# Kernel optimization log

Measured on AMD Instinct MI355X. Metric: run time of the kernel, lower is better.

The kernel has to match this reference:

```python
import jax, jax.numpy as jnp
import numpy as np

N = 48
E = N * (N - 1)
H_LSTM = 32
EPS = 20.0

def _conv1d(x, w, b):
    # x: [B, Cin, L], w: [Cout, Cin, K] -> [B, Cout, L], 'same' padding
    y = jax.lax.conv_general_dilated(x, w, window_strides=(1,), padding='SAME',
                                     dimension_numbers=('NCH', 'OIH', 'NCH'))
    return y + b[None, :, None]

def _map(M, x):
    # map_features: linear map along dim 0 (gather for n_to_e one-hot rows,
    # incidence-sum scatter for e_to_n). M: [O, I], x: [I, ...] -> [O, ...]
    return jnp.tensordot(M, x, axes=1)

def _node_cnn(x, adj, layers, final):
    # graph conv stack: neighbor mix (adj along dim 0) + conv1d over node axis + relu
    nl = len(layers)
    for i, (w, b) in enumerate(layers):
        x = _conv1d(_map(adj, x), w, b)
        if not (final and i == nl - 1):
            x = jax.nn.relu(x)
    return x

def _node_lstm(x, mem, adj, w, b):
    # mem = cat([c, h], dim=1); gates from conv over adj-mixed cat([x, h])
    H = mem.shape[1] // 2
    c, h = mem[:, :H], mem[:, H:]
    gates = _conv1d(_map(adj, jnp.concatenate([x, h], axis=1)), w, b)
    i, f, g, o = jnp.split(gates, 4, axis=1)
    c2 = jax.nn.sigmoid(f) * c + jax.nn.sigmoid(i) * jnp.tanh(g)
    h2 = jax.nn.sigmoid(o) * jnp.tanh(c2)
    return jnp.concatenate([c2, h2], axis=1)

def _forward(bi, bij, msgi, msgj, v, nmem0, emem0, neadj, eeadj,
             e_to_n0, e_to_n1, n_to_e0, n_to_e1, decoding, params):
    fm, efm, nlstm, elstm, pp, epp = params
    n = bi.shape[0]
    e = bij.shape[0]
    # map_node_feature_to_edge
    bi_g1 = _map(n_to_e0, bi)   # [E,1,N]
    bi_g2 = _map(n_to_e1, bi)   # [E,1,N]
    # softmax (logsumexp) message computation over bij [E,1,N,N]
    cmsgi = jax.nn.logsumexp((bi_g2[:, :, None, :] + bij) * EPS, axis=3) / EPS  # [E,1,N]
    cmsgj = jax.nn.logsumexp((bi_g1[:, :, :, None] + bij) * EPS, axis=2) / EPS  # [E,1,N]
    ncmsgi = _map(e_to_n0, cmsgi)
    ncmsgj = _map(e_to_n1, cmsgj)
    nnmsgi = _map(e_to_n0, msgi)
    nnmsgj = _map(e_to_n1, msgj)
    # partial_feature (detached in original)
    dec_mat = jax.nn.one_hot(decoding, n, dtype=bi.dtype)        # [N,N]
    xi = _map(n_to_e0, dec_mat)[:, :, None]                      # [E,N,1]
    xj = _map(n_to_e1, dec_mat)[:, None, :]                      # [E,1,N]
    ep = bij.reshape(e, n, n)
    f1 = jax.lax.stop_gradient(_map(e_to_n0, (ep * xi).sum(axis=1)).reshape(n, 1, n))
    f2 = jax.lax.stop_gradient(_map(e_to_n1, (ep * xj).sum(axis=2)).reshape(n, 1, n))
    node_feature = jnp.concatenate([bi, bi + v, nnmsgi, nnmsgj, ncmsgi, ncmsgj, f1, f2], axis=1)  # [N,8,N]
    edge_feature = jnp.concatenate([msgi, msgj, cmsgi, cmsgj, bi_g1, bi_g2], axis=1)              # [E,6,N]
    nfeat = _node_cnn(node_feature, neadj, fm, False)   # [N,32,N]
    efeat = _node_cnn(edge_feature, eeadj, efm, False)  # [E,32,N]
    ntoe1, ntoe2 = _map(n_to_e0, nfeat), _map(n_to_e1, nfeat)
    eton1, eton2 = _map(e_to_n0, efeat), _map(e_to_n1, efeat)
    nfeat = jnp.concatenate([nfeat, eton1, eton2], axis=1)  # [N,96,N]
    efeat = jnp.concatenate([efeat, ntoe1, ntoe2], axis=1)  # [E,96,N]
    nmem_new = _node_lstm(nfeat, nmem0, neadj, nlstm[0], nlstm[1])  # [N,64,N]
    emem_new = _node_lstm(efeat, emem0, eeadj, elstm[0], elstm[1])  # [E,64,N]
    nfeat = nmem_new[:, H_LSTM:]   # h part
    efeat = emem_new[:, H_LSTM:]
    ntoe1, ntoe2 = _map(n_to_e0, nfeat), _map(n_to_e1, nfeat)
    eton1, eton2 = _map(e_to_n0, efeat), _map(e_to_n1, efeat)
    nfeat = jnp.concatenate([nfeat, eton1, eton2], axis=1)
    efeat = jnp.concatenate([efeat, ntoe1, ntoe2], axis=1)
    efeat = _node_cnn(efeat, eeadj, epp, True)   # [E,2,N]
    nfeat = _node_cnn(nfeat, neadj, pp, True)    # [N,1,N]
    nmsgi = efeat[:, 0:1] + 0.5 * cmsgi - msgi
    nmsgj = efeat[:, 1:2] + 0.5 * cmsgj - msgj
    nv = nfeat.mean(axis=0, keepdims=True)       # [1,1,N]
    v_out = v + nv
    bij_out = bij - nmsgi.reshape(e, 1, n, 1) - nmsgj.reshape(e, 1, 1, n)
    bi_out = bi + _map(e_to_n0, nmsgi) + _map(e_to_n1, nmsgj) - nv
    msgi_out = msgi + nmsgi
    msgj_out = msgj + nmsgj
    # get_current_dual (softmax=True)
    cdual = (v_out.sum()
             + jax.nn.logsumexp(bi_out.reshape(-1, n) * EPS, axis=1).sum() / EPS
             + jax.nn.logsumexp(bij_out.reshape(-1, n * n) * EPS, axis=1).sum() / EPS)
    return bi_out, bij_out, msgi_out, msgj_out, v_out, cdual, nmem_new, emem_new, f1, f2

def setup_inputs() -> dict:
    key = jax.random.key(0)
    ks = jax.random.split(key, 16)
    ii, jj = np.meshgrid(np.arange(N), np.arange(N), indexing='ij')
    mask = ii != jj
    src, dst = ii[mask], jj[mask]  # [E] complete directed graph
    eye = np.eye(N, dtype=np.float32)
    n_to_e0 = jnp.asarray(eye[src])  # [E,N] one-hot gather
    n_to_e1 = jnp.asarray(eye[dst])
    e_to_n0 = n_to_e0.T              # [N,E] incidence scatter-sum
    e_to_n1 = n_to_e1.T
    def glorot(k, shape):
        fan_in = shape[1] * shape[2]
        return jax.random.normal(k, shape, jnp.float32) / np.sqrt(fan_in)
    pk = jax.random.split(ks[15], 20)
    return dict(
        bi=jax.random.normal(ks[0], (N, 1, N), jnp.float32),
        bij=jax.random.normal(ks[1], (E, 1, N, N), jnp.float32),
        msgi=jnp.zeros((E, 1, N), jnp.float32),
        msgj=jnp.zeros((E, 1, N), jnp.float32),
        v=jnp.zeros((1, 1, N), jnp.float32),
        nmem0=jnp.zeros((N, 2 * H_LSTM, N), jnp.float32),
        emem0=jnp.zeros((E, 2 * H_LSTM, N), jnp.float32),
        neadj=jax.random.uniform(ks[2], (N, N), jnp.float32) / N,
        eeadj=jax.random.uniform(ks[3], (E, E), jnp.float32) / E,
        e_to_n0=e_to_n0, e_to_n1=e_to_n1, n_to_e0=n_to_e0, n_to_e1=n_to_e1,
        decoding=jax.random.randint(ks[4], (N,), 0, N),
        fm_w0=glorot(pk[0], (32, 8, 3)), fm_b0=jnp.zeros((32,), jnp.float32),
        fm_w1=glorot(pk[1], (32, 32, 3)), fm_b1=jnp.zeros((32,), jnp.float32),
        efm_w0=glorot(pk[2], (32, 6, 3)), efm_b0=jnp.zeros((32,), jnp.float32),
        efm_w1=glorot(pk[3], (32, 32, 3)), efm_b1=jnp.zeros((32,), jnp.float32),
        nlstm_w=glorot(pk[4], (128, 128, 3)), nlstm_b=jnp.zeros((128,), jnp.float32),
        elstm_w=glorot(pk[5], (128, 128, 3)), elstm_b=jnp.zeros((128,), jnp.float32),
        pp_w0=glorot(pk[6], (16, 96, 3)), pp_b0=jnp.zeros((16,), jnp.float32),
        pp_w1=glorot(pk[7], (1, 16, 3)), pp_b1=jnp.zeros((1,), jnp.float32),
        epp_w0=glorot(pk[8], (16, 96, 3)), epp_b0=jnp.zeros((16,), jnp.float32),
        epp_w1=glorot(pk[9], (2, 16, 3)), epp_b1=jnp.zeros((2,), jnp.float32),
    )

def reference(bi, bij, msgi, msgj, v, nmem0, emem0, neadj, eeadj,
              e_to_n0, e_to_n1, n_to_e0, n_to_e1, decoding,
              fm_w0, fm_b0, fm_w1, fm_b1, efm_w0, efm_b0, efm_w1, efm_b1,
              nlstm_w, nlstm_b, elstm_w, elstm_b,
              pp_w0, pp_b0, pp_w1, pp_b1, epp_w0, epp_b0, epp_w1, epp_b1):
    params = ([(fm_w0, fm_b0), (fm_w1, fm_b1)],
              [(efm_w0, efm_b0), (efm_w1, efm_b1)],
              (nlstm_w, nlstm_b), (elstm_w, elstm_b),
              [(pp_w0, pp_b0), (pp_w1, pp_b1)],
              [(epp_w0, epp_b0), (epp_w1, epp_b1)])
    return _forward(bi, bij, msgi, msgj, v, nmem0, emem0, neadj, eeadj,
                    e_to_n0, e_to_n1, n_to_e0, n_to_e1, decoding, params)
```

## Files before the change

kernel.cpp:

```cpp
#include <hip/hip_runtime.h>
#include <cstdint>
#include <cstddef>

#define EE 2256
#define EP 2304

typedef __attribute__((ext_vector_type(8))) short bf16x8;
typedef __attribute__((ext_vector_type(4))) float f32x4;

__device__ __forceinline__ unsigned short f2b(float f){
  unsigned u = __builtin_bit_cast(unsigned, f);
  u += 0x7fffu + ((u>>16)&1u);
  return (unsigned short)(u>>16);
}
__device__ __forceinline__ float b2f(unsigned short h){
  unsigned u = ((unsigned)h)<<16; return __builtin_bit_cast(float, u);
}
__device__ __forceinline__ float sigm(float x){ return 1.f/(1.f+__expf(-x)); }
__device__ __forceinline__ float tanhfast(float x){ return 1.f - 2.f/(__expf(2.f*x)+1.f); }

typedef __attribute__((address_space(3))) unsigned int lds_u32;
typedef __attribute__((address_space(1))) const unsigned int gbl_u32;
__device__ __forceinline__ void glds16(const void* g, void* l){
  __builtin_amdgcn_global_load_lds((gbl_u32*)g, (lds_u32*)l, 16, 0, 0);
}

__global__ void gm_zero(float4* p, long n){
  long i = (long)blockIdx.x*blockDim.x + threadIdx.x;
  if (i < n) p[i] = make_float4(0.f,0.f,0.f,0.f);
}

__global__ void gm_prep_eeadj(const float* __restrict__ src, unsigned short* __restrict__ dst){
  int idx = blockIdx.x*256 + threadIdx.x;
  if (idx >= EP*EP) return;
  int r = idx / EP, k = idx - r*EP;
  float v = (r < EE && k < EE) ? src[(size_t)r*EE + k] : 0.f;
  dst[idx] = f2b(v);
}

__global__ void gm_prep_wconv(const float* __restrict__ w, unsigned short* __restrict__ dst,
                              int Co, int Cin, int KPT, int Kpad, int tot){
  int idx = blockIdx.x*256 + threadIdx.x;
  if (idx >= tot) return;
  int co = idx / Kpad; int k = idx - co*Kpad;
  int t = k / KPT; int ci = k - t*KPT;
  float v = (co < Co && t < 3 && ci < Cin) ? w[((size_t)co*Cin + ci)*3 + t] : 0.f;
  dst[idx] = f2b(v);
}

__global__ __launch_bounds__(256) void gm_cmsg(const float* __restrict__ bi, const float* __restrict__ bij,
                                               float* __restrict__ cmi, float* __restrict__ cmj){
  int e = blockIdx.x; int tid = threadIdx.x;
  __shared__ float t[48*49]; __shared__ float bs[48], bd[48];
  const float* src = bij + (size_t)e*2304;
  for (int i=tid;i<2304;i+=256){ int r=i/48, c=i-r*48; t[r*49+c]=src[i]; }
  if (tid<48){ int s=e/47, m=e-s*47; int d=m+(m>=s); bs[tid]=bi[s*48+tid]; bd[tid]=bi[d*48+tid]; }
  __syncthreads();
  if (tid < 48){
    float mx=-1e30f;
    for (int n=0;n<48;n++) mx = fmaxf(mx, t[tid*49+n]+bd[n]);
    float sm=0.f;
    for (int n=0;n<48;n++) sm += __expf((t[tid*49+n]+bd[n]-mx)*20.f);
    cmi[e*48+tid] = mx + __logf(sm)*(1.f/20.f);
  } else if (tid>=64 && tid<112){
    int n = tid-64;
    float mx=-1e30f;
    for (int k=0;k<48;k++) mx = fmaxf(mx, t[k*49+n]+bs[k]);
    float sm=0.f;
    for (int k=0;k<48;k++) sm += __expf((t[k*49+n]+bs[k]-mx)*20.f);
    cmj[e*48+n] = mx + __logf(sm)*(1.f/20.f);
  }
}

__global__ __launch_bounds__(256) void gm_node_accum(const float* __restrict__ bij, const float* __restrict__ cmi,
                              const float* __restrict__ cmj, const float* __restrict__ msgi,
                              const float* __restrict__ msgj, const int* __restrict__ dec,
                              float* ncmi, float* ncmj, float* nnmi, float* nnmj,
                              float* o_f1, float* o_f2){
  int i = blockIdx.x; int tid = threadIdx.x;
  __shared__ float red[5][6][48];
  int mg = tid / 48;
  int w  = tid - mg*48;
  if (mg < 5){
    int dc = dec[i];
    float a1=0,a2=0,a3=0,a4=0,s1=0,s2=0;
    for (int m=mg; m<47; m+=5){
      int e1 = i*47+m;
      a1 += cmi[e1*48+w]; a3 += msgi[e1*48+w];
      s1 += bij[(size_t)e1*2304 + dc*48 + w];
      int j = m + (m>=i); int e2 = j*47 + i - (i>j);
      a2 += cmj[e2*48+w]; a4 += msgj[e2*48+w];
      s2 += bij[(size_t)e2*2304 + w*48 + dc];
    }
    red[mg][0][w]=a1; red[mg][1][w]=a2; red[mg][2][w]=a3;
    red[mg][3][w]=a4; red[mg][4][w]=s1; red[mg][5][w]=s2;
  }
  __syncthreads();
  if (tid < 48){
    float a1=0,a2=0,a3=0,a4=0,s1=0,s2=0;
    for (int g=0; g<5; g++){
      a1+=red[g][0][tid]; a2+=red[g][1][tid]; a3+=red[g][2][tid];
      a4+=red[g][3][tid]; s1+=red[g][4][tid]; s2+=red[g][5][tid];
    }
    ncmi[i*48+tid]=a1; ncmj[i*48+tid]=a2; nnmi[i*48+tid]=a3; nnmj[i*48+tid]=a4;
    o_f1[i*48+tid]=s1; o_f2[i*48+tid]=s2;
  }
}

__global__ void gm_build_x6(const float* __restrict__ msgi, const float* __restrict__ msgj,
                            const float* __restrict__ cmi, const float* __restrict__ cmj,
                            const float* __restrict__ bi, unsigned short* __restrict__ x6){
  int idx = blockIdx.x*256 + threadIdx.x;
  if (idx >= 6*EP) return;
  int c = idx / EP, e = idx - c*EP;
  if (e >= EE){ for (int w=0;w<48;w++) x6[(size_t)(w*6+c)*EP + e] = 0; return; }
  int s = e/47, m = e-s*47, d = m + (m>=s);
  for (int w=0; w<48; w++){
    float x;
    switch(c){
      case 0: x = msgi[e*48+w]; break;
      case 1: x = msgj[e*48+w]; break;
      case 2: x = cmi[e*48+w]; break;
      case 3: x = cmj[e*48+w]; break;
      case 4: x = bi[s*48+w]; break;
      default: x = bi[d*48+w]; break;
    }
    x6[(size_t)(w*6+c)*EP + e] = f2b(x);
  }
}

__global__ void gm_fill_x128_hi(const float* __restrict__ emem0, const float* __restrict__ nfeat,
                                unsigned short* __restrict__ x128){
  int idx = blockIdx.x*256 + threadIdx.x;
  if (idx >= 96*EP) return;
  int q = idx/EP; int c = 32 + q; int e = idx - q*EP;
  if (e >= EE){ for (int w=0;w<48;w++) x128[(size_t)(w*128+c)*EP + e] = 0; return; }
  int s=e/47, m=e-s*47, d=m+(m>=s);
  const float* srcrow;
  if (c < 64)      srcrow = nfeat + ((size_t)s*32 + (c-32))*48;
  else if (c < 96) srcrow = nfeat + ((size_t)d*32 + (c-64))*48;
  else             srcrow = emem0 + ((size_t)e*64 + (c-64))*48;
  #pragma unroll
  for (int w4=0; w4<12; w4++){
    float4 xv = *(const float4*)(srcrow + w4*4);
    x128[(size_t)((w4*4+0)*128+c)*EP + e] = f2b(xv.x);
    x128[(size_t)((w4*4+1)*128+c)*EP + e] = f2b(xv.y);
    x128[(size_t)((w4*4+2)*128+c)*EP + e] = f2b(xv.z);
    x128[(size_t)((w4*4+3)*128+c)*EP + e] = f2b(xv.w);
  }
}

__global__ __launch_bounds__(256) void gm_map_gemm(
    const unsigned short* __restrict__ A, const unsigned short* __restrict__ BT,
    unsigned short* __restrict__ ypad, float* __restrict__ outf,
    const float* __restrict__ bias, int Nvalid, int Cch, int Cslab, int do_relu, int f32_out)
{
  __shared__ __align__(16) unsigned short lA[128*32];
  __shared__ __align__(16) unsigned short lB[128*32];
  const int tid = threadIdx.x;
  const int lane = tid & 63, wid = tid >> 6;
  const int m0 = blockIdx.x * 128;
  const int n0 = blockIdx.y * 128;
  const int wm = wid >> 1, wn = wid & 1;
  f32x4 acc[4][4];
  #pragma unroll
  for (int i=0;i<4;i++){
    #pragma unroll
    for (int j=0;j<4;j++) acc[i][j] = f32x4{0.f,0.f,0.f,0.f};
  }
  const int srow = (lane>>2), scol = (lane&3);

  for (int ks = 0; ks < EP/32; ++ks) {
    #pragma unroll
    for (int q=0;q<2;q++){
      int chunk = wid*2+q;
      int row = chunk*16 + srow;
      int off = (scol*16) ^ (((row>>1)&3)<<4);
      glds16((const char*)A  + (size_t)(m0+row)*(EP*2) + ks*64 + off, (char*)lA + chunk*1024);
      glds16((const char*)BT + (size_t)(n0+row)*(EP*2) + ks*64 + off, (char*)lB + chunk*1024);
    }
    __syncthreads();
    bf16x8 af[4], bfr[4];
    #pragma unroll
    for (int mi=0;mi<4;mi++){
      int row = wm*64 + mi*16 + (lane&15);
      int off = ((lane>>4)*16) ^ (((row>>1)&3)<<4);
      af[mi] = *(const bf16x8*)((const char*)lA + row*64 + off);
    }
    #pragma unroll
    for (int ni=0;ni<4;ni++){
      int row = wn*64 + ni*16 + (lane&15);
      int off = ((lane>>4)*16) ^ (((row>>1)&3)<<4);
      bfr[ni] = *(const bf16x8*)((const char*)lB + row*64 + off);
    }
    #pragma unroll
    for (int mi=0;mi<4;mi++){
      #pragma unroll
      for (int ni=0;ni<4;ni++)
        acc[mi][ni] = __builtin_amdgcn_mfma_f32_16x16x32_bf16(af[mi], bfr[ni], acc[mi][ni], 0,0,0);
    }
    __syncthreads();
  }
  #pragma unroll
  for (int mi=0;mi<4;mi++){
    int ebase = m0 + wm*64 + mi*16 + (lane>>4)*4;
    #pragma unroll
    for (int ni=0;ni<4;ni++){
      int c = n0 + wn*64 + ni*16 + (lane&15);
      if (c >= Nvalid) continue;
      int w = c / Cch, ci = c - w*Cch;
      float bv = bias ? bias[ci] : 0.f;
      #pragma unroll
      for (int r=0;r<4;r++){
        int e = ebase + r;
        if (e >= EE) continue;
        float x = acc[mi][ni][r] + bv;
        if (do_relu) x = fmaxf(x, 0.f);
        if (f32_out) outf[(size_t)e*Nvalid + c] = x;
        else ypad[((size_t)e*50 + 1 + w)*Cslab + ci] = f2b(x);
      }
    }
  }
}

template<int BM>
__global__ __launch_bounds__(256) void gm_conv_gemm(
    const unsigned short* __restrict__ Wp, const unsigned short* __restrict__ ypad,
    unsigned short* __restrict__ outT, const float* __restrict__ bias,
    int Cch, int KPT, int Kpad, int Co, int Ct, int do_relu)
{
  constexpr int MI = (BM==128)?4:((BM==32)?2:1);
  constexpr int NI = (BM==128)?4:2;
  __shared__ __align__(16) unsigned short lA[BM*32];
  __shared__ __align__(16) unsigned short lB[128*32];
  const int tid = threadIdx.x, lane = tid&63, wid = tid>>6;
  const int e0 = blockIdx.x * 128;
  const int w  = blockIdx.y;
  const int rowb = (BM==128)? (wid>>1)*64 : 0;
  const int colb = (BM==128)? (wid&1)*64 : wid*32;
  f32x4 acc[MI][NI];
  #pragma unroll
  for (int i=0;i<MI;i++){
    #pragma unroll
    for (int j=0;j<NI;j++) acc[i][j] = f32x4{0.f,0.f,0.f,0.f};
  }
  const int srow=(lane>>2), scol=(lane&3);
  const int ksteps = Kpad/32;
  for (int ks=0; ks<ksteps; ++ks){
    for (int c = wid; c < BM/16; c += 4){
      int row = c*16 + srow;
      int off = (scol*16) ^ (((row>>1)&3)<<4);
      glds16((const char*)Wp + (size_t)row*(Kpad*2) + ks*64 + off, (char*)lA + c*1024);
    }
    for (int c = wid; c < 8; c += 4){
      int row = c*16 + srow;
      int off = (scol*16) ^ (((row>>1)&3)<<4);
      int kg = ks*32 + (off>>1);
      int t = kg / KPT;
      int ci = kg - t*KPT;
      int e = e0 + row;
      const char* src;
      if (t < 3 && e < EE) src = (const char*)ypad + ((size_t)(e*50 + w + t)*Cch + ci)*2;
      else                 src = (const char*)ypad;
      glds16(src, (char*)lB + c*1024);
    }
    __syncthreads();
    bf16x8 af[MI], bfr[NI];
    #pragma unroll
    for (int mi=0;mi<MI;mi++){
      int row = rowb + mi*16 + (lane&15);
      int off = ((lane>>4)*16) ^ (((row>>1)&3)<<4);
      af[mi] = *(const bf16x8*)((const char*)lA + row*64 + off);
    }
    #pragma unroll
    for (int ni=0;ni<NI;ni++){
      int row = colb + ni*16 + (lane&15);
      int off = ((lane>>4)*16) ^ (((row>>1)&3)<<4);
      bfr[ni] = *(const bf16x8*)((const char*)lB + row*64 + off);
    }
    #pragma unroll
    for (int mi=0;mi<MI;mi++){
      #pragma unroll
      for (int ni=0;ni<NI;ni++)
        acc[mi][ni] = __builtin_amdgcn_mfma_f32_16x16x32_bf16(af[mi], bfr[ni], acc[mi][ni], 0,0,0);
    }
    __syncthreads();
  }
  #pragma unroll
  for (int mi=0;mi<MI;mi++){
    #pragma unroll
// ... 18 lines not shown
                            const float* __restrict__ ncmi, const float* __restrict__ ncmj,
                            const float* __restrict__ f1, const float* __restrict__ f2,
                            float* __restrict__ nf){
  int idx = blockIdx.x*256+threadIdx.x;
  if (idx >= 48*8*48) return;
  int i = idx/(8*48); int rem = idx - i*(8*48); int c = rem/48; int w = rem-c*48;
  int iw = i*48+w;
  float x;
  switch(c){
    case 0: x=bi[iw]; break;
    case 1: x=bi[iw]+v[w]; break;
    case 2: x=nnmi[iw]; break;
    case 3: x=nnmj[iw]; break;
    case 4: x=ncmi[iw]; break;
    case 5: x=ncmj[iw]; break;
    case 6: x=f1[iw]; break;
    default: x=f2[iw]; break;
  }
  nf[idx]=x;
}

__global__ void gm_nmap(const float* __restrict__ adj, const float* __restrict__ X,
                        float* __restrict__ Y, int C){
  int idx = blockIdx.x*256 + threadIdx.x;
  int tot = 48*C*48;
  if (idx >= tot) return;
  int i = idx/(C*48); int rem = idx - i*(C*48);
  float s=0.f;
  for (int j=0;j<48;j++) s += adj[i*48+j]*X[(size_t)j*C*48 + rem];
  Y[idx]=s;
}

__global__ void gm_nconv(const float* __restrict__ X, const float* __restrict__ wgt,
                         const float* __restrict__ bias, float* __restrict__ Y,
                         int Cin, int Co, int relu){
  int idx = blockIdx.x*256 + threadIdx.x;
  int tot = 48*Co*48;
  if (idx >= tot) return;
  int i = idx/(Co*48); int rem = idx - i*(Co*48); int co = rem/48; int w = rem-co*48;
  float s = bias[co];
  const float* xb = X + (size_t)i*Cin*48;
  const float* wb = wgt + (size_t)co*Cin*3;
  for (int ci=0; ci<Cin; ++ci){
    float w0 = wb[ci*3], w1 = wb[ci*3+1], w2 = wb[ci*3+2];
    const float* xr = xb + ci*48;
    if (w > 0) s += xr[w-1]*w0;
    s += xr[w]*w1;
    if (w < 47) s += xr[w+1]*w2;
  }
  if (relu) s = fmaxf(s, 0.f);
  Y[idx] = s;
}

__global__ void gm_build_xnode(const float* __restrict__ nfeat, const unsigned short* __restrict__ x128,
                               const float* __restrict__ nmem0, float* __restrict__ xn){
  int idx = blockIdx.x*256 + threadIdx.x;
  if (idx >= 48*128*48) return;
  int i = idx/(128*48); int rem = idx - i*(128*48); int c = rem/48; int w = rem - c*48;
  float s;
  if (c < 32) s = nfeat[((size_t)i*32+c)*48+w];
  else if (c < 96){
    int cc = (c-32) & 31; bool issrc = (c<64);
    float a = 0.f;
    for (int m=0;m<47;m++){
      int e;
      if (issrc) e = i*47+m;
      else { int j = m + (m>=i); e = j*47 + i - (i>j); }
      a += b2f(x128[(size_t)(w*128+cc)*EP + e]);
    }
    s = a;
  } else s = nmem0[((size_t)i*64 + (c-64))*48 + w];
  xn[idx] = s;
}

__global__ void gm_nlstm_pw(const float* __restrict__ gates, const float* __restrict__ nmem0,
                            float* __restrict__ o_nmem, float* __restrict__ nfeat2){
  int idx = blockIdx.x*256 + threadIdx.x;
  if (idx >= 48*32*48) return;
  int i = idx/(32*48); int rem = idx - i*(32*48); int ch = rem/48; int w = rem-ch*48;
  float gi = gates[((size_t)i*128 + ch)*48 + w];
  float gf = gates[((size_t)i*128 + 32+ch)*48 + w];
  float gg = gates[((size_t)i*128 + 64+ch)*48 + w];
  float go = gates[((size_t)i*128 + 96+ch)*48 + w];
  float c  = nmem0[((size_t)i*64 + ch)*48 + w];
  float c2 = sigm(gf)*c + sigm(gi)*tanhfast(gg);
  float h2 = sigm(go)*tanhfast(c2);
  o_nmem[((size_t)i*64 + ch)*48 + w] = c2;
  o_nmem[((size_t)i*64 + 32+ch)*48 + w] = h2;
  nfeat2[((size_t)i*32 + ch)*48 + w] = h2;
}

__global__ __launch_bounds__(256) void gm_elstm_pw(const unsigned short* __restrict__ gatesT,
                                                   const float* __restrict__ emem0,
                                                   float* __restrict__ o_emem){
  int bid = blockIdx.x;
  int e4 = bid / 6, chunk = bid - e4*6;
  int cw = chunk*256 + threadIdx.x;
  int ch = cw / 48, w = cw - ch*48;
  int ebase = e4*4;
  const unsigned short* g0 = gatesT + (size_t)(w*128 + ch)*EP + ebase;
  ushort4 vi = *(const ushort4*)(g0);
  ushort4 vf = *(const ushort4*)(g0 + (size_t)32*EP);
  ushort4 vg = *(const ushort4*)(g0 + (size_t)64*EP);
  ushort4 vo = *(const ushort4*)(g0 + (size_t)96*EP);
  const unsigned short* pi = (const unsigned short*)&vi;
  const unsigned short* pf = (const unsigned short*)&vf;
  const unsigned short* pg = (const unsigned short*)&vg;
  const unsigned short* po = (const unsigned short*)&vo;
  #pragma unroll
  for (int r=0;r<4;r++){
    int e = ebase + r;
    float gi = b2f(pi[r]), gf = b2f(pf[r]), gg = b2f(pg[r]), go = b2f(po[r]);
    float c  = emem0[((size_t)e*64 + ch)*48 + w];
    float c2 = sigm(gf)*c + sigm(gi)*tanhfast(gg);
    float h2 = sigm(go)*tanhfast(c2);
    o_emem[((size_t)e*64 + ch)*48 + w] = c2;
    o_emem[((size_t)e*64 + 32+ch)*48 + w] = h2;
  }
}

__global__ __launch_bounds__(128) void gm_build_xpp(const float* __restrict__ o_emem,
                                                    const float* __restrict__ nfeat2,
                                                    unsigned short* __restrict__ xpp){
  int e = blockIdx.x; int tid = threadIdx.x;
  __shared__ float h[1536];
  const float* src = o_emem + ((size_t)e*64 + 32)*48;
  for (int i=tid;i<1536;i+=128) h[i]=src[i];
  if (tid < 96){
    xpp[((size_t)e*50 + 0)*96 + tid] = 0;
    xpp[((size_t)e*50 + 49)*96 + tid] = 0;
  }
  __syncthreads();
  int s = e/47; int m = e - s*47; int d = m + (m>=s);
  for (int w=0; w<48; w++){
    if (tid < 96){
      float x;
      if (tid<32) x = h[tid*48+w];
      else if (tid<64) x = nfeat2[((size_t)s*32 + tid-32)*48 + w];
      else x = nfeat2[((size_t)d*32 + tid-64)*48 + w];
      xpp[((size_t)e*50 + 1 + w)*96 + tid] = f2b(x);
    }
  }
}

__global__ void gm_build_x2(const float* __restrict__ nfeat2, const float* __restrict__ o_emem,
                            float* __restrict__ x2){
  int idx = blockIdx.x*256 + threadIdx.x;
  if (idx >= 48*96*48) return;
  int i = idx/(96*48); int rem = idx - i*(96*48); int c = rem/48; int w = rem - c*48;
  float s;
  if (c<32) s = nfeat2[((size_t)i*32+c)*48+w];
  else {
    int cc = (c-32)&31; bool issrc = (c<64);
    float a=0.f;
    for (int m=0;m<47;m++){
      int e;
      if (issrc) e = i*47+m;
      else { int j = m + (m>=i); e = j*47 + i - (i>j); }
      a += o_emem[((size_t)e*64 + 32 + cc)*48 + w];
    }
    s=a;
  }
  x2[idx]=s;
}

__global__ void gm_nv(const float* __restrict__ nfpp, const float* __restrict__ v,
                      float* __restrict__ nv, float* __restrict__ o_v){
  int w = threadIdx.x;
  if (w<48){
    float s=0.f; for (int i=0;i<48;i++) s += nfpp[i*48+w];
    s *= (1.f/48.f);
    nv[w]=s; o_v[w]=v[w]+s;
  }
}

__global__ void gm_nmsg(const float* __restrict__ effpp, const float* __restrict__ cmi,
                        const float* __restrict__ cmj, const float* __restrict__ msgi,
                        const float* __restrict__ msgj, float* __restrict__ nmi,
                        float* __restrict__ nmj, float* __restrict__ o_mi, float* __restrict__ o_mj){
  int idx = blockIdx.x*256 + threadIdx.x;
  if (idx >= EE*48) return;
  int e = idx/48, w = idx-e*48;
  float a = effpp[(size_t)e*96 + w*2]     + 0.5f*cmi[idx] - msgi[idx];
  float b = effpp[(size_t)e*96 + w*2 + 1] + 0.5f*cmj[idx] - msgj[idx];
  nmi[idx]=a; nmj[idx]=b;
  o_mi[idx]=msgi[idx]+a; o_mj[idx]=msgj[idx]+b;
}

__global__ __launch_bounds__(256) void gm_bijout(const float* __restrict__ bij,
                                                 const float* __restrict__ nmi, const float* __restrict__ nmj,
                                                 float* __restrict__ o_bij, float* __restrict__ lse_e){
  int e = blockIdx.x; int tid = threadIdx.x;
  __shared__ float ri[48], rj[48], red[8];
  if (tid < 48) ri[tid] = nmi[e*48+tid];
  else if (tid >= 64 && tid < 112) rj[tid-64] = nmj[e*48+tid-64];
  __syncthreads();
  float v[9]; float mx = -1e30f;
  const float* src = bij + (size_t)e*2304;
  float* dst = o_bij + (size_t)e*2304;
  #pragma unroll
  for (int q=0;q<9;q++){
    int idx = q*256 + tid;
    int r = idx/48, c = idx-r*48;
    float x = src[idx] - ri[r] - rj[c];
    dst[idx] = x; v[q] = x; mx = fmaxf(mx, x);
  }
  for (int o=1;o<64;o<<=1) mx = fmaxf(mx, __shfl_xor(mx, o, 64));
  int lane = tid&63, w4 = tid>>6;
  if (lane==0) red[w4] = mx;
  __syncthreads();
  mx = fmaxf(fmaxf(red[0],red[1]),fmaxf(red[2],red[3]));
  float s = 0.f;
  #pragma unroll
  for (int q=0;q<9;q++) s += __expf((v[q]-mx)*20.f);
  for (int o=1;o<64;o<<=1) s += __shfl_xor(s, o, 64);
  if (lane==0) red[4+w4] = s;
  __syncthreads();
  if (tid==0){
    float t = red[4]+red[5]+red[6]+red[7];
    lse_e[e] = mx + __logf(t)*(1.f/20.f);
  }
}

__global__ void gm_biout(const float* __restrict__ bi, const float* __restrict__ nmi,
                         const float* __restrict__ nmj, const float* __restrict__ nv,
                         float* __restrict__ o_bi, float* __restrict__ lse_n){
  int i = blockIdx.x; int w = threadIdx.x;
  float val = -1e30f;
  if (w < 48){
    float s = 0.f;
    for (int m=0;m<47;m++){
      int e1 = i*47+m;
      s += nmi[e1*48+w];
      int j = m + (m>=i);
      int e2 = j*47 + i - (i>j);
      s += nmj[e2*48+w];
    }
    val = bi[i*48+w] + s - nv[w];
    o_bi[i*48+w] = val;
  }
  float mx = val;
  for (int o=1;o<64;o<<=1) mx = fmaxf(mx, __shfl_xor(mx, o, 64));
  float ex = (w<48)? __expf((val-mx)*20.f) : 0.f;
  for (int o=1;o<64;o<<=1) ex += __shfl_xor(ex, o, 64);
  if (w==0) lse_n[i] = mx + __logf(ex)*(1.f/20.f);
}

__global__ void gm_cdual(const float* __restrict__ lse_e, const float* __restrict__ lse_n,
// ... 66 lines not shown
  const float* epp_w0= (const float*)d_in[30]; const float* epp_b0= (const float*)d_in[31];
  const float* epp_w1= (const float*)d_in[32]; const float* epp_b1= (const float*)d_in[33];

  char* ws = (char*)d_ws;
  unsigned short* eeadjb = (unsigned short*)(ws + OFF_EEADJ);
  unsigned short* x6t    = (unsigned short*)(ws + OFF_X6T);
  unsigned short* x32t   = (unsigned short*)(ws + OFF_X32T);
  unsigned short* x128t  = (unsigned short*)(ws + OFF_X128T);
  unsigned short* z1t    = x32t;
  unsigned short* z2t    = x6t;
  unsigned short* gatesT = x128t;
  unsigned short* yp6    = (unsigned short*)(ws + OFF_YP6);
  unsigned short* yp32   = (unsigned short*)(ws + OFF_YP32);
  unsigned short* yp128  = (unsigned short*)(ws + OFF_YP128);
  unsigned short* yp16   = (unsigned short*)(ws + OFF_YP16);
  unsigned short* xpp    = (unsigned short*)(ws + OFF_XPP);
  unsigned short* wc0 = (unsigned short*)(ws + OFF_WC0);
  unsigned short* wc1 = (unsigned short*)(ws + OFF_WC1);
  unsigned short* wcl = (unsigned short*)(ws + OFF_WCL);
  unsigned short* wp0 = (unsigned short*)(ws + OFF_WP0);
  unsigned short* wp1 = (unsigned short*)(ws + OFF_WP1);
  float* cmi  = (float*)(ws + OFF_CMI);
  float* cmj  = (float*)(ws + OFF_CMJ);
  float* nmi  = (float*)(ws + OFF_NMI);
  float* nmj  = (float*)(ws + OFF_NMJ);
  float* effpp= (float*)(ws + OFF_EFPP);
  float* lse_e= (float*)(ws + OFF_LSEE);
  float* lse_n= (float*)(ws + OFF_LSEN);
  float* nvb  = (float*)(ws + OFF_NV);
  float* nf   = (float*)(ws + OFF_NF);
  float* nt1  = (float*)(ws + OFF_NT1);
  float* nt2  = (float*)(ws + OFF_NT2);
  float* nfeat  = (float*)(ws + OFF_NFEAT);
  float* nfeat2 = (float*)(ws + OFF_NFEAT2);
  float* xn   = (float*)(ws + OFF_XN);
  float* nfpp = (float*)(ws + OFF_NFPP);
  float* ncmi = (float*)(ws + OFF_NAC);
  float* ncmj = ncmi + 2304;
  float* nnmi = ncmi + 2*2304;
  float* nnmj = ncmi + 3*2304;

  float* out = (float*)d_out;
  float* o_bi   = out;
  float* o_bij  = out + 2304;
  float* o_mi   = out + 2304 + 5197824;
  float* o_mj   = o_mi + 108288;
  float* o_v    = o_mj + 108288;
  float* o_cd   = o_v + 48;
  float* o_nmem = o_cd + 1;
  float* o_emem = o_nmem + 147456;
  float* o_f1   = o_emem + 6930432;
  float* o_f2   = o_f1 + 2304;

  {
    long n = (long)((OFF_ZEND - OFF_YP6)/16);
    gm_zero<<<(unsigned)((n+255)/256), 256, 0, stream>>>((float4*)(ws+OFF_YP6), n);
  }
  gm_prep_eeadj<<<(EP*EP+255)/256, 256, 0, stream>>>(eeadj, eeadjb);
  gm_prep_wconv<<<(32*32+255)/256,  256, 0, stream>>>(efm_w0, wc0, 32,6,8,32,   32*32);
  gm_prep_wconv<<<(32*96+255)/256,  256, 0, stream>>>(efm_w1, wc1, 32,32,32,96, 32*96);
  gm_prep_wconv<<<(128*384+255)/256,256, 0, stream>>>(el_w,   wcl, 128,128,128,384, 128*384);
  gm_prep_wconv<<<(16*288+255)/256, 256, 0, stream>>>(epp_w0, wp0, 16,96,96,288, 16*288);
  gm_prep_wconv<<<(16*64+255)/256,  256, 0, stream>>>(epp_w1, wp1, 2,16,16,64,  16*64);
  gm_cmsg<<<EE, 256, 0, stream>>>(bi, bij, cmi, cmj);
  gm_node_accum<<<48, 256, 0, stream>>>(bij, cmi, cmj, msgi, msgj, dec, ncmi, ncmj, nnmi, nnmj, o_f1, o_f2);
  gm_build_x6<<<(6*EP+255)/256, 256, 0, stream>>>(msgi, msgj, cmi, cmj, bi, x6t);
  gm_build_nf<<<(48*8*48+255)/256, 256, 0, stream>>>(bi, v_in, nnmi, nnmj, ncmi, ncmj, o_f1, o_f2, nf);
  gm_nmap<<<(48*8*48+255)/256, 256, 0, stream>>>(neadj, nf, nt1, 8);
  gm_nconv<<<(48*32*48+255)/256, 256, 0, stream>>>(nt1, fm_w0, fm_b0, nt2, 8, 32, 1);
  gm_nmap<<<(48*32*48+255)/256, 256, 0, stream>>>(neadj, nt2, nt1, 32);
  gm_nconv<<<(48*32*48+255)/256, 256, 0, stream>>>(nt1, fm_w1, fm_b1, nfeat, 32, 32, 1);
  gm_map_gemm<<<dim3(18,3),  256, 0, stream>>>(eeadjb, x6t,  yp6,  nullptr, nullptr, 288, 6, 8, 0, 0);
  gm_conv_gemm<32><<<dim3(18,48), 256, 0, stream>>>(wc0, yp6,  x32t, efm_b0, 8, 8, 32, 32, 32, 1);
  gm_map_gemm<<<dim3(18,12), 256, 0, stream>>>(eeadjb, x32t, yp32, nullptr, nullptr, 1536, 32, 32, 0, 0);
  gm_conv_gemm<32><<<dim3(18,48), 256, 0, stream>>>(wc1, yp32, x128t, efm_b1, 32, 32, 96, 32, 128, 1);
  gm_fill_x128_hi<<<(96*EP+255)/256, 256, 0, stream>>>(emem0, nfeat, x128t);
  gm_build_xnode<<<(48*128*48+255)/256, 256, 0, stream>>>(nfeat, x128t, nmem0, xn);
  gm_nmap<<<(48*128*48+255)/256, 256, 0, stream>>>(neadj, xn, nt1, 128);
  gm_nconv<<<(48*128*48+255)/256, 256, 0, stream>>>(nt1, nl_w, nl_b, nt2, 128, 128, 0);
  gm_nlstm_pw<<<(48*32*48+255)/256, 256, 0, stream>>>(nt2, nmem0, o_nmem, nfeat2);
  gm_map_gemm<<<dim3(18,48), 256, 0, stream>>>(eeadjb, x128t, yp128, nullptr, nullptr, 6144, 128, 128, 0, 0);
  gm_conv_gemm<128><<<dim3(18,48), 256, 0, stream>>>(wcl, yp128, gatesT, el_b, 128, 128, 384, 128, 128, 0);
  gm_elstm_pw<<<564*6, 256, 0, stream>>>(gatesT, emem0, o_emem);
  gm_build_xpp<<<EE, 128, 0, stream>>>(o_emem, nfeat2, xpp);
  gm_conv_gemm<16><<<dim3(18,48), 256, 0, stream>>>(wp0, xpp,  z1t, nullptr, 96, 96, 288, 16, 16, 0);
  gm_map_gemm<<<dim3(18,6), 256, 0, stream>>>(eeadjb, z1t, yp16, nullptr, epp_b0, 768, 16, 16, 1, 0);
  gm_conv_gemm<16><<<dim3(18,48), 256, 0, stream>>>(wp1, yp16, z2t, nullptr, 16, 16, 64, 2, 2, 0);
  gm_map_gemm<<<dim3(18,1), 256, 0, stream>>>(eeadjb, z2t, nullptr, effpp, epp_b1, 96, 2, 2, 0, 1);
  gm_build_x2<<<(48*96*48+255)/256, 256, 0, stream>>>(nfeat2, o_emem, xn);
  gm_nmap<<<(48*96*48+255)/256, 256, 0, stream>>>(neadj, xn, nt1, 96);
  gm_nconv<<<(48*16*48+255)/256, 256, 0, stream>>>(nt1, pp_w0, pp_b0, nt2, 96, 16, 1);
  gm_nmap<<<(48*16*48+255)/256, 256, 0, stream>>>(neadj, nt2, nt1, 16);
  gm_nconv<<<(48*1*48+255)/256, 256, 0, stream>>>(nt1, pp_w1, pp_b1, nfpp, 16, 1, 0);
  gm_nv<<<1, 64, 0, stream>>>(nfpp, v_in, nvb, o_v);
  gm_nmsg<<<(EE*48+255)/256, 256, 0, stream>>>(effpp, cmi, cmj, msgi, msgj, nmi, nmj, o_mi, o_mj);
  gm_bijout<<<EE, 256, 0, stream>>>(bij, nmi, nmj, o_bij, lse_e);
  gm_biout<<<48, 64, 0, stream>>>(bi, nmi, nmj, nvb, o_bi, lse_n);
  gm_cdual<<<1, 256, 0, stream>>>(lse_e, lse_n, o_v, o_cd);
}
```

Measured before the change: 970.7 us.

## Fuse small kernels, swizzle GEMM blocks across XCDs, restructure edge-to-node sums

Several independent changes go in together. The five weight-prep launches merge into one, and the full workspace zero is replaced by zeroing only the pad rows. The node conv is fused with the LSTM pointwise step, and the message update is folded into the bij output kernel. GEMM grids become 1D with an XCD-aware swizzle so neighbouring tiles share an L2. The edge-to-node gathers are rewritten as row-per-block reductions staged through LDS, which replaces strided per-thread loops. The fused node LSTM conv now does four times the work per thread, which may lower parallelism.

```diff
diff --git a/kernel.cpp b/kernel.cpp
--- a/kernel.cpp
+++ b/kernel.cpp
@@ -19,15 +19,29 @@
 __device__ __forceinline__ float sigm(float x){ return 1.f/(1.f+__expf(-x)); }
 __device__ __forceinline__ float tanhfast(float x){ return 1.f - 2.f/(__expf(2.f*x)+1.f); }
 
+__device__ __forceinline__ int xcd_swz(int bid, int nwg){
+  int xcd = bid & 7, idx = bid >> 3;
+  int q = nwg >> 3, r = nwg & 7;
+  return (xcd < r ? xcd*(q+1) : r*(q+1) + (xcd-r)*q) + idx;
+}
+
 typedef __attribute__((address_space(3))) unsigned int lds_u32;
 typedef __attribute__((address_space(1))) const unsigned int gbl_u32;
 __device__ __forceinline__ void glds16(const void* g, void* l){
   __builtin_amdgcn_global_load_lds((gbl_u32*)g, (lds_u32*)l, 16, 0, 0);
 }
 
-__global__ void gm_zero(float4* p, long n){
-  long i = (long)blockIdx.x*blockDim.x + threadIdx.x;
-  if (i < n) p[i] = make_float4(0.f,0.f,0.f,0.f);
+__global__ __launch_bounds__(128) void gm_zero_pads(unsigned short* yp6, unsigned short* yp32,
+                                                    unsigned short* yp128, unsigned short* yp16){
+  int e = blockIdx.x; int tid = threadIdx.x;
+  #pragma unroll
+  for (int r=0; r<2; ++r){
+    int row = r ? 49 : 0;
+    if (tid < 8)  yp6 [((size_t)e*50+row)*8  + tid] = 0;
+    if (tid < 32) yp32[((size_t)e*50+row)*32 + tid] = 0;
+    yp128[((size_t)e*50+row)*128 + tid] = 0;
+    if (tid < 16) yp16[((size_t)e*50+row)*16 + tid] = 0;
+  }
 }
 
 __global__ void gm_prep_eeadj(const float* __restrict__ src, unsigned short* __restrict__ dst){
@@ -38,22 +52,31 @@
   dst[idx] = f2b(v);
 }
 
-__global__ void gm_prep_wconv(const float* __restrict__ w, unsigned short* __restrict__ dst,
-                              int Co, int Cin, int KPT, int Kpad, int tot){
+__global__ void gm_prep_wall(const float* __restrict__ w0, const float* __restrict__ w1,
+                             const float* __restrict__ w2, const float* __restrict__ w3,
+                             const float* __restrict__ w4,
+                             unsigned short* d0, unsigned short* d1, unsigned short* d2,
+                             unsigned short* d3, unsigned short* d4){
   int idx = blockIdx.x*256 + threadIdx.x;
-  if (idx >= tot) return;
-  int co = idx / Kpad; int k = idx - co*Kpad;
+  const float* w; unsigned short* dp; int Co,Cin,KPT,Kpad,loc;
+  if      (idx < 1024) { w=w0; dp=d0; Co=32;  Cin=6;   KPT=8;   Kpad=32;  loc=idx; }
+  else if (idx < 4096) { w=w1; dp=d1; Co=32;  Cin=32;  KPT=32;  Kpad=96;  loc=idx-1024; }
+  else if (idx < 53248){ w=w2; dp=d2; Co=128; Cin=128; KPT=128; Kpad=384; loc=idx-4096; }
+  else if (idx < 57856){ w=w3; dp=d3; Co=16;  Cin=96;  KPT=96;  Kpad=288; loc=idx-53248; }
+  else if (idx < 58880){ w=w4; dp=d4; Co=2;   Cin=16;  KPT=16;  Kpad=64;  loc=idx-57856; }
+  else return;
+  int co = loc / Kpad; int k = loc - co*Kpad;
   int t = k / KPT; int ci = k - t*KPT;
   float v = (co < Co && t < 3 && ci < Cin) ? w[((size_t)co*Cin + ci)*3 + t] : 0.f;
-  dst[idx] = f2b(v);
-}
-
-__global__ __launch_bounds__(256) void gm_cmsg(const float* __restrict__ bi, const float* __restrict__ bij,
+  dp[loc] = f2b(v);
+}
+
+__global__ __launch_bounds__(128) void gm_cmsg(const float* __restrict__ bi, const float* __restrict__ bij,
                                                float* __restrict__ cmi, float* __restrict__ cmj){
   int e = blockIdx.x; int tid = threadIdx.x;
   __shared__ float t[48*49]; __shared__ float bs[48], bd[48];
   const float* src = bij + (size_t)e*2304;
-  for (int i=tid;i<2304;i+=256){ int r=i/48, c=i-r*48; t[r*49+c]=src[i]; }
+  for (int i=tid;i<2304;i+=128){ int r=i/48, c=i-r*48; t[r*49+c]=src[i]; }
   if (tid<48){ int s=e/47, m=e-s*47; int d=m+(m>=s); bs[tid]=bi[s*48+tid]; bd[tid]=bi[d*48+tid]; }
   __syncthreads();
   if (tid < 48){
@@ -153,14 +176,15 @@
 __global__ __launch_bounds__(256) void gm_map_gemm(
     const unsigned short* __restrict__ A, const unsigned short* __restrict__ BT,
     unsigned short* __restrict__ ypad, float* __restrict__ outf,
-    const float* __restrict__ bias, int Nvalid, int Cch, int Cslab, int do_relu, int f32_out)
+    const float* __restrict__ bias, int ncol, int Nvalid, int Cch, int Cslab, int do_relu, int f32_out)
 {
   __shared__ __align__(16) unsigned short lA[128*32];
   __shared__ __align__(16) unsigned short lB[128*32];
   const int tid = threadIdx.x;
   const int lane = tid & 63, wid = tid >> 6;
-  const int m0 = blockIdx.x * 128;
-  const int n0 = blockIdx.y * 128;
+  const int swz = xcd_swz(blockIdx.x, gridDim.x);
+  const int m0 = (swz / ncol) * 128;
+  const int n0 = (swz % ncol) * 128;
   const int wm = wid >> 1, wn = wid & 1;
   f32x4 acc[4][4];
   #pragma unroll
@@ -234,8 +258,9 @@
   __shared__ __align__(16) unsigned short lA[BM*32];
   __shared__ __align__(16) unsigned short lB[128*32];
   const int tid = threadIdx.x, lane = tid&63, wid = tid>>6;
-  const int e0 = blockIdx.x * 128;
-  const int w  = blockIdx.y;
+  const int swz = xcd_swz(blockIdx.x, 864);
+  const int e0 = (swz / 48) * 128;
+  const int w  = swz % 48;
   const int rowb = (BM==128)? (wid>>1)*64 : 0;
   const int colb = (BM==128)? (wid&1)*64 : wid*32;
   f32x4 acc[MI][NI];
@@ -360,42 +385,66 @@
   Y[idx] = s;
 }
 
-__global__ void gm_build_xnode(const float* __restrict__ nfeat, const unsigned short* __restrict__ x128,
-                               const float* __restrict__ nmem0, float* __restrict__ xn){
-  int idx = blockIdx.x*256 + threadIdx.x;
-  if (idx >= 48*128*48) return;
-  int i = idx/(128*48); int rem = idx - i*(128*48); int c = rem/48; int w = rem - c*48;
-  float s;
-  if (c < 32) s = nfeat[((size_t)i*32+c)*48+w];
-  else if (c < 96){
-    int cc = (c-32) & 31; bool issrc = (c<64);
-    float a = 0.f;
-    for (int m=0;m<47;m++){
-      int e;
-      if (issrc) e = i*47+m;
-      else { int j = m + (m>=i); e = j*47 + i - (i>j); }
-      a += b2f(x128[(size_t)(w*128+cc)*EP + e]);
-    }
-    s = a;
-  } else s = nmem0[((size_t)i*64 + (c-64))*48 + w];
-  xn[idx] = s;
-}
-
-__global__ void gm_nlstm_pw(const float* __restrict__ gates, const float* __restrict__ nmem0,
-                            float* __restrict__ o_nmem, float* __restrict__ nfeat2){
+__global__ __launch_bounds__(256) void gm_nconv_lstm(const float* __restrict__ X,
+    const float* __restrict__ wgt, const float* __restrict__ bias,
+    const float* __restrict__ nmem0, float* __restrict__ o_nmem, float* __restrict__ nfeat2){
   int idx = blockIdx.x*256 + threadIdx.x;
   if (idx >= 48*32*48) return;
   int i = idx/(32*48); int rem = idx - i*(32*48); int ch = rem/48; int w = rem-ch*48;
-  float gi = gates[((size_t)i*128 + ch)*48 + w];
-  float gf = gates[((size_t)i*128 + 32+ch)*48 + w];
-  float gg = gates[((size_t)i*128 + 64+ch)*48 + w];
-  float go = gates[((size_t)i*128 + 96+ch)*48 + w];
-  float c  = nmem0[((size_t)i*64 + ch)*48 + w];
-  float c2 = sigm(gf)*c + sigm(gi)*tanhfast(gg);
-  float h2 = sigm(go)*tanhfast(c2);
-  o_nmem[((size_t)i*64 + ch)*48 + w] = c2;
-  o_nmem[((size_t)i*64 + 32+ch)*48 + w] = h2;
-  nfeat2[((size_t)i*32 + ch)*48 + w] = h2;
+  const float* xb = X + (size_t)i*128*48;
+  float s0=bias[ch], s1=bias[32+ch], s2=bias[64+ch], s3=bias[96+ch];
+  for (int ci=0; ci<128; ++ci){
+    const float* xr = xb + ci*48;
+    float xm = (w>0)? xr[w-1] : 0.f;
+    float xc = xr[w];
+    float xp = (w<47)? xr[w+1] : 0.f;
+    const float* wb0 = wgt + ((size_t)ch*128+ci)*3;
+    const float* wb1 = wgt + ((size_t)(32+ch)*128+ci)*3;
+    const float* wb2 = wgt + ((size_t)(64+ch)*128+ci)*3;
+    const float* wb3 = wgt + ((size_t)(96+ch)*128+ci)*3;
+    s0 += xm*wb0[0]+xc*wb0[1]+xp*wb0[2];
+    s1 += xm*wb1[0]+xc*wb1[1]+xp*wb1[2];
+    s2 += xm*wb2[0]+xc*wb2[1]+xp*wb2[2];
+    s3 += xm*wb3[0]+xc*wb3[1]+xp*wb3[2];
+  }
+  float c = nmem0[((size_t)i*64+ch)*48+w];
+  float c2 = sigm(s1)*c + sigm(s0)*tanhfast(s2);
+  float h2 = sigm(s3)*tanhfast(c2);
+  o_nmem[((size_t)i*64+ch)*48+w] = c2;
+  o_nmem[((size_t)i*64+32+ch)*48+w] = h2;
+  nfeat2[((size_t)i*32+ch)*48+w] = h2;
+}
+
+__global__ __launch_bounds__(256) void gm_eton_x128(const unsigned short* __restrict__ x128,
+                                                    float* __restrict__ xn){
+  int row = blockIdx.x;
+  int w = row >> 5, cc = row & 31;
+  __shared__ float L[2256];
+  const unsigned short* src = x128 + (size_t)(w*128 + cc)*EP;
+  for (int t=threadIdx.x; t<2256; t+=256) L[t] = b2f(src[t]);
+  __syncthreads();
+  int tid = threadIdx.x;
+  if (tid < 48){
+    int i = tid; float s=0.f;
+    for (int m=0;m<47;m++) s += L[i*47+m];
+    xn[((size_t)i*128 + 32 + cc)*48 + w] = s;
+  } else if (tid >= 64 && tid < 112){
+    int i = tid-64; float s=0.f;
+    for (int m=0;m<47;m++){
+      int j = m + (m>=i);
+      s += L[j*47 + i - (i>j)];
+    }
+    xn[((size_t)i*128 + 64 + cc)*48 + w] = s;
+  }
+}
+
+__global__ void gm_xnode_copy(const float* __restrict__ nfeat, const float* __restrict__ nmem0,
+                              float* __restrict__ xn){
+  int idx = blockIdx.x*256+threadIdx.x;
+  if (idx >= 48*64*48) return;
+  int i = idx/(64*48); int rem = idx - i*(64*48); int c = rem/48; int w = rem-c*48;
+  if (c < 32) xn[((size_t)i*128 + c)*48 + w] = nfeat[((size_t)i*32+c)*48+w];
+  else        xn[((size_t)i*128 + 96 + (c-32))*48 + w] = nmem0[((size_t)i*64 + 32 + (c-32))*48 + w];
 }
 
 __global__ __launch_bounds__(256) void gm_elstm_pw(const unsigned short* __restrict__ gatesT,
@@ -427,49 +476,57 @@
   }
 }
 
+__global__ __launch_bounds__(256) void gm_eton_h(const float* __restrict__ o_emem,
+                                                 float* __restrict__ x2){
+  int row = blockIdx.x; int w = row >> 5, cc = row & 31;
+  __shared__ float L[2256];
+  for (int t=threadIdx.x; t<2256; t+=256)
+    L[t] = o_emem[((size_t)t*64 + 32 + cc)*48 + w];
+  __syncthreads();
+  int tid = threadIdx.x;
+  if (tid < 48){
+    int i=tid; float s=0.f;
+    for (int m=0;m<47;m++) s += L[i*47+m];
+    x2[((size_t)i*96 + 32 + cc)*48 + w] = s;
+  } else if (tid>=64 && tid<112){
+    int i=tid-64; float s=0.f;
+    for (int m=0;m<47;m++){ int j=m+(m>=i); s += L[j*47 + i - (i>j)]; }
+    x2[((size_t)i*96 + 64 + cc)*48 + w] = s;
+  }
+}
+
+__global__ void gm_x2_copy(const float* __restrict__ nfeat2, float* __restrict__ x2){
+  int idx = blockIdx.x*256+threadIdx.x;
+  if (idx >= 48*32*48) return;
+  int i = idx/(32*48); int rem = idx - i*(32*48); int c = rem/48; int w = rem-c*48;
+  x2[((size_t)i*96 + c)*48 + w] = nfeat2[idx];
+}
+
 __global__ __launch_bounds__(128) void gm_build_xpp(const float* __restrict__ o_emem,
                                                     const float* __restrict__ nfeat2,
                                                     unsigned short* __restrict__ xpp){
   int e = blockIdx.x; int tid = threadIdx.x;
   __shared__ float h[1536];
+  __shared__ float sn[3072];
+  int s = e/47; int m = e - s*47; int d = m + (m>=s);
   const float* src = o_emem + ((size_t)e*64 + 32)*48;
   for (int i=tid;i<1536;i+=128) h[i]=src[i];
+  const float* ps = nfeat2 + (size_t)s*32*48;
+  const float* pd = nfeat2 + (size_t)d*32*48;
+  for (int i=tid;i<1536;i+=128){ sn[i]=ps[i]; sn[1536+i]=pd[i]; }
   if (tid < 96){
     xpp[((size_t)e*50 + 0)*96 + tid] = 0;
     xpp[((size_t)e*50 + 49)*96 + tid] = 0;
   }
   __syncthreads();
-  int s = e/47; int m = e - s*47; int d = m + (m>=s);
   for (int w=0; w<48; w++){
     if (tid < 96){
       float x;
       if (tid<32) x = h[tid*48+w];
-      else if (tid<64) x = nfeat2[((size_t)s*32 + tid-32)*48 + w];
-      else x = nfeat2[((size_t)d*32 + tid-64)*48 + w];
+      else x = sn[(tid-32)*48 + w];
       xpp[((size_t)e*50 + 1 + w)*96 + tid] = f2b(x);
     }
   }
-}
-
-__global__ void gm_build_x2(const float* __restrict__ nfeat2, const float* __restrict__ o_emem,
-                            float* __restrict__ x2){
-  int idx = blockIdx.x*256 + threadIdx.x;
-  if (idx >= 48*96*48) return;
-  int i = idx/(96*48); int rem = idx - i*(96*48); int c = rem/48; int w = rem - c*48;
-  float s;
-  if (c<32) s = nfeat2[((size_t)i*32+c)*48+w];
-  else {
-    int cc = (c-32)&31; bool issrc = (c<64);
-    float a=0.f;
-    for (int m=0;m<47;m++){
-      int e;
-      if (issrc) e = i*47+m;
-      else { int j = m + (m>=i); e = j*47 + i - (i>j); }
-      a += o_emem[((size_t)e*64 + 32 + cc)*48 + w];
-    }
-    s=a;
-  }
-  x2[idx]=s;
 }
 
 __global__ void gm_nv(const float* __restrict__ nfpp, const float* __restrict__ v,
@@ -482,26 +539,24 @@
   }
 }
 
-__global__ void gm_nmsg(const float* __restrict__ effpp, const float* __restrict__ cmi,
-                        const float* __restrict__ cmj, const float* __restrict__ msgi,
-                        const float* __restrict__ msgj, float* __restrict__ nmi,
-                        float* __restrict__ nmj, float* __restrict__ o_mi, float* __restrict__ o_mj){
-  int idx = blockIdx.x*256 + threadIdx.x;
-  if (idx >= EE*48) return;
-  int e = idx/48, w = idx-e*48;
-  float a = effpp[(size_t)e*96 + w*2]     + 0.5f*cmi[idx] - msgi[idx];
-  float b = effpp[(size_t)e*96 + w*2 + 1] + 0.5f*cmj[idx] - msgj[idx];
-  nmi[idx]=a; nmj[idx]=b;
-  o_mi[idx]=msgi[idx]+a; o_mj[idx]=msgj[idx]+b;
-}
-
 __global__ __launch_bounds__(256) void gm_bijout(const float* __restrict__ bij,
-                                                 const float* __restrict__ nmi, const float* __restrict__ nmj,
+                                                 const float* __restrict__ effpp,
+                                                 const float* __restrict__ cmi, const float* __restrict__ cmj,
+                                                 const float* __restrict__ msgi, const float* __restrict__ msgj,
+                                                 float* __restrict__ nmi, float* __restrict__ nmj,
+                                                 float* __restrict__ o_mi, float* __restrict__ o_mj,
                                                  float* __restrict__ o_bij, float* __restrict__ lse_e){
   int e = blockIdx.x; int tid = threadIdx.x;
   __shared__ float ri[48], rj[48], red[8];
-  if (tid < 48) ri[tid] = nmi[e*48+tid];
-  else if (tid >= 64 && tid < 112) rj[tid-64] = nmj[e*48+tid-64];
+  if (tid < 48){
+    int idx = e*48+tid;
+    float a = effpp[(size_t)e*96 + tid*2] + 0.5f*cmi[idx] - msgi[idx];
+    ri[tid] = a; nmi[idx] = a; o_mi[idx] = msgi[idx] + a;
+  } else if (tid >= 64 && tid < 112){
+    int t2 = tid-64; int idx = e*48+t2;
+    float b = effpp[(size_t)e*96 + t2*2 + 1] + 0.5f*cmj[idx] - msgj[idx];
+    rj[t2] = b; nmj[idx] = b; o_mj[idx] = msgj[idx] + b;
+  }
   __syncthreads();
   float v[9]; float mx = -1e30f;
   const float* src = bij + (size_t)e*2304;
@@ -674,17 +729,11 @@
   float* o_f1   = o_emem + 6930432;
   float* o_f2   = o_f1 + 2304;
 
-  {
-    long n = (long)((OFF_ZEND - OFF_YP6)/16);
-    gm_zero<<<(unsigned)((n+255)/256), 256, 0, stream>>>((float4*)(ws+OFF_YP6), n);
-  }
+  gm_zero_pads<<<EE, 128, 0, stream>>>(yp6, yp32, yp128, yp16);
   gm_prep_eeadj<<<(EP*EP+255)/256, 256, 0, stream>>>(eeadj, eeadjb);
-  gm_prep_wconv<<<(32*32+255)/256,  256, 0, stream>>>(efm_w0, wc0, 32,6,8,32,   32*32);
-  gm_prep_wconv<<<(32*96+255)/256,  256, 0, stream>>>(efm_w1, wc1, 32,32,32,96, 32*96);
-  gm_prep_wconv<<<(128*384+255)/256,256, 0, stream>>>(el_w,   wcl, 128,128,128,384, 128*384);
-  gm_prep_wconv<<<(16*288+255)/256, 256, 0, stream>>>(epp_w0, wp0, 16,96,96,288, 16*288);
-  gm_prep_wconv<<<(16*64+255)/256,  256, 0, stream>>>(epp_w1, wp1, 2,16,16,64,  16*64);
-  gm_cmsg<<<EE, 256, 0, stream>>>(bi, bij, cmi, cmj);
+  gm_prep_wall<<<(58880+255)/256, 256, 0, stream>>>(efm_w0, efm_w1, el_w, epp_w0, epp_w1,
+                                                    wc0, wc1, wcl, wp0, wp1);
+  gm_cmsg<<<EE, 128, 0, stream>>>(bi, bij, cmi, cmj);
   gm_node_accum<<<48, 256, 0, stream>>>(bij, cmi, cmj, msgi, msgj, dec, ncmi, ncmj, nnmi, nnmj, o_f1, o_f2);
   gm_build_x6<<<(6*EP+255)/256, 256, 0, stream>>>(msgi, msgj, cmi, cmj, bi, x6t);
   gm_build_nf<<<(48*8*48+255)/256, 256, 0, stream>>>(bi, v_in, nnmi, nnmj, ncmi, ncmj, o_f1, o_f2, nf);
@@ -692,31 +741,31 @@
   gm_nconv<<<(48*32*48+255)/256, 256, 0, stream>>>(nt1, fm_w0, fm_b0, nt2, 8, 32, 1);
   gm_nmap<<<(48*32*48+255)/256, 256, 0, stream>>>(neadj, nt2, nt1, 32);
   gm_nconv<<<(48*32*48+255)/256, 256, 0, stream>>>(nt1, fm_w1, fm_b1, nfeat, 32, 32, 1);
-  gm_map_gemm<<<dim3(18,3),  256, 0, stream>>>(eeadjb, x6t,  yp6,  nullptr, nullptr, 288, 6, 8, 0, 0);
-  gm_conv_gemm<32><<<dim3(18,48), 256, 0, stream>>>(wc0, yp6,  x32t, efm_b0, 8, 8, 32, 32, 32, 1);
-  gm_map_gemm<<<dim3(18,12), 256, 0, stream>>>(eeadjb, x32t, yp32, nullptr, nullptr, 1536, 32, 32, 0, 0);
-  gm_conv_gemm<32><<<dim3(18,48), 256, 0, stream>>>(wc1, yp32, x128t, efm_b1, 32, 32, 96, 32, 128, 1);
+  gm_map_gemm<<<54,  256, 0, stream>>>(eeadjb, x6t,  yp6,  nullptr, nullptr, 3, 288, 6, 8, 0, 0);
+  gm_conv_gemm<32><<<864, 256, 0, stream>>>(wc0, yp6,  x32t, efm_b0, 8, 8, 32, 32, 32, 1);
+  gm_map_gemm<<<216, 256, 0, stream>>>(eeadjb, x32t, yp32, nullptr, nullptr, 12, 1536, 32, 32, 0, 0);
+  gm_conv_gemm<32><<<864, 256, 0, stream>>>(wc1, yp32, x128t, efm_b1, 32, 32, 96, 32, 128, 1);
   gm_fill_x128_hi<<<(96*EP+255)/256, 256, 0, stream>>>(emem0, nfeat, x128t);
-  gm_build_xnode<<<(48*128*48+255)/256, 256, 0, stream>>>(nfeat, x128t, nmem0, xn);
+  gm_xnode_copy<<<(48*64*48+255)/256, 256, 0, stream>>>(nfeat, nmem0, xn);
+  gm_eton_x128<<<1536, 256, 0, stream>>>(x128t, xn);
   gm_nmap<<<(48*128*48+255)/256, 256, 0, stream>>>(neadj, xn, nt1, 128);
-  gm_nconv<<<(48*128*48+255)/256, 256, 0, stream>>>(nt1, nl_w, nl_b, nt2, 128, 128, 0);
-  gm_nlstm_pw<<<(48*32*48+255)/256, 256, 0, stream>>>(nt2, nmem0, o_nmem, nfeat2);
-  gm_map_gemm<<<dim3(18,48), 256, 0, stream>>>(eeadjb, x128t, yp128, nullptr, nullptr, 6144, 128, 128, 0, 0);
-  gm_conv_gemm<128><<<dim3(18,48), 256, 0, stream>>>(wcl, yp128, gatesT, el_b, 128, 128, 384, 128, 128, 0);
+  gm_nconv_lstm<<<(48*32*48+255)/256, 256, 0, stream>>>(nt1, nl_w, nl_b, nmem0, o_nmem, nfeat2);
+  gm_map_gemm<<<864, 256, 0, stream>>>(eeadjb, x128t, yp128, nullptr, nullptr, 48, 6144, 128, 128, 0, 0);
+  gm_conv_gemm<128><<<864, 256, 0, stream>>>(wcl, yp128, gatesT, el_b, 128, 128, 384, 128, 128, 0);
   gm_elstm_pw<<<564*6, 256, 0, stream>>>(gatesT, emem0, o_emem);
   gm_build_xpp<<<EE, 128, 0, stream>>>(o_emem, nfeat2, xpp);
-  gm_conv_gemm<16><<<dim3(18,48), 256, 0, stream>>>(wp0, xpp,  z1t, nullptr, 96, 96, 288, 16, 16, 0);
-  gm_map_gemm<<<dim3(18,6), 256, 0, stream>>>(eeadjb, z1t, yp16, nullptr, epp_b0, 768, 16, 16, 1, 0);
-  gm_conv_gemm<16><<<dim3(18,48), 256, 0, stream>>>(wp1, yp16, z2t, nullptr, 16, 16, 64, 2, 2, 0);
-  gm_map_gemm<<<dim3(18,1), 256, 0, stream>>>(eeadjb, z2t, nullptr, effpp, epp_b1, 96, 2, 2, 0, 1);
-  gm_build_x2<<<(48*96*48+255)/256, 256, 0, stream>>>(nfeat2, o_emem, xn);
+  gm_conv_gemm<16><<<864, 256, 0, stream>>>(wp0, xpp,  z1t, nullptr, 96, 96, 288, 16, 16, 0);
+  gm_map_gemm<<<108, 256, 0, stream>>>(eeadjb, z1t, yp16, nullptr, epp_b0, 6, 768, 16, 16, 1, 0);
+  gm_conv_gemm<16><<<864, 256, 0, stream>>>(wp1, yp16, z2t, nullptr, 16, 16, 64, 2, 2, 0);
+  gm_map_gemm<<<18, 256, 0, stream>>>(eeadjb, z2t, nullptr, effpp, epp_b1, 1, 96, 2, 2, 0, 1);
+  gm_x2_copy<<<(48*32*48+255)/256, 256, 0, stream>>>(nfeat2, xn);
+  gm_eton_h<<<1536, 256, 0, stream>>>(o_emem, xn);
   gm_nmap<<<(48*96*48+255)/256, 256, 0, stream>>>(neadj, xn, nt1, 96);
   gm_nconv<<<(48*16*48+255)/256, 256, 0, stream>>>(nt1, pp_w0, pp_b0, nt2, 96, 16, 1);
   gm_nmap<<<(48*16*48+255)/256, 256, 0, stream>>>(neadj, nt2, nt1, 16);
   gm_nconv<<<(48*1*48+255)/256, 256, 0, stream>>>(nt1, pp_w1, pp_b1, nfpp, 16, 1, 0);
   gm_nv<<<1, 64, 0, stream>>>(nfpp, v_in, nvb, o_v);
-  gm_nmsg<<<(EE*48+255)/256, 256, 0, stream>>>(effpp, cmi, cmj, msgi, msgj, nmi, nmj, o_mi, o_mj);
-  gm_bijout<<<EE, 256, 0, stream>>>(bij, nmi, nmj, o_bij, lse_e);
+  gm_bijout<<<EE, 256, 0, stream>>>(bij, effpp, cmi, cmj, msgi, msgj, nmi, nmj, o_mi, o_mj, o_bij, lse_e);
   gm_biout<<<48, 64, 0, stream>>>(bi, nmi, nmj, nvb, o_bi, lse_n);
   gm_cdual<<<1, 256, 0, stream>>>(lse_e, lse_n, o_v, o_cd);
 }
```

Result: faster. 876.7 us (-9.7%).
